# Optimization experiments

Hardware: AMD Instinct MI355X
Metric: run time of the kernel (lower is better)

The kernel has to match this reference:

```python
import jax, jax.numpy as jnp
import numpy as np

N, T, H, W, C = 64, 32, 64, 64, 256
HID, NB, P, OUT = 512, 12, 7, 388
CIN = P * P + 2  # 49 patch values + 2 normalized coords


def _ln(x, s):
    # haiku LayerNorm(axis=-1, create_scale=True, create_offset=False), eps=1e-5
    m = jnp.mean(x, axis=-1, keepdims=True)
    v = jnp.var(x, axis=-1, keepdims=True)
    return (x - m) * jax.lax.rsqrt(v + 1e-5) * s


def _dwconv(x, w, b, groups):
    # hk.DepthwiseConv1D, NWC, stride 1, SAME padding; w: [K, 1, C_out]
    y = jax.lax.conv_general_dilated(
        x, w, (1,), 'SAME', dimension_numbers=('NWC', 'WIO', 'NWC'),
        feature_group_count=groups)
    return y + b


def _forward(feature_grid, query_feats, pos, in_w, in_b, dw1_w, dw1_b, dw2_w,
             dw2_b, ln1_s, ln2_s, up_w, up_b, down_w, down_b, lnf_s, out_w,
             out_b):
    pad = P - 1
    # cost volume: einsum('bnc,bthwc->tbnhw') with batch=1, laid out [N,T,H,W]
    corrs = jnp.einsum('nc,thwc->nthw', query_feats, feature_grid)
    padded = jnp.pad(corrs, ((0, 0), (0, 0), (pad, pad), (pad, pad)))
    # extract_patch_depthwise_conv: the separable bilinear bump kernel convolved
    # VALID over the padded map equals a bilinear sample at (o + pos + P/2 - 1).
    pp = pos + P / 2.0 - 1.0  # [N,T,2] (y,x)
    iy = jnp.floor(pp[..., 0])
    ix = jnp.floor(pp[..., 1])
    fy = (pp[..., 0] - iy)[..., None, None]
    fx = (pp[..., 1] - ix)[..., None, None]
    offs = jnp.arange(P, dtype=jnp.int32)
    y0 = iy.astype(jnp.int32)[..., None] + offs  # [N,T,P]
    x0 = ix.astype(jnp.int32)[..., None] + offs  # [N,T,P]
    gat = jax.vmap(jax.vmap(lambda img, yi, xi: img[yi][:, xi]))
    patch = ((1 - fy) * (1 - fx) * gat(padded, y0, x0)
             + (1 - fy) * fx * gat(padded, y0, x0 + 1)
             + fy * (1 - fx) * gat(padded, y0 + 1, x0)
             + fy * fx * gat(padded, y0 + 1, x0 + 1))  # [N,T,P,P]
    x = jnp.concatenate(
        [patch.reshape(patch.shape[0], patch.shape[1], P * P),
         pos / jnp.float32(H)], axis=-1)  # [N,T,CIN]
    # PIPSMLPMixer
    x = x @ in_w + in_b  # [N,T,HID]
    for i in range(NB):
        # PIPsConvBlock: depthwise_conv_residual
        skip = x
        h = _ln(x, ln1_s[i])
        h = jax.nn.gelu(_dwconv(h, dw1_w[i], dw1_b[i], HID))  # ch mult 4
        h = _dwconv(h, dw2_w[i], dw2_b[i], HID * 4)           # ch mult 1
        h = h[..., 0::4] + h[..., 1::4] + h[..., 2::4] + h[..., 3::4]
        x = h + skip
        # conv_channels_mixer
        skip = x
        h = _ln(x, ln2_s[i])
        h = jax.nn.gelu(h @ up_w[i] + up_b[i]) @ down_w[i] + down_b[i]
        x = h + skip
    x = _ln(x, lnf_s)
    return x @ out_w + out_b  # [N,T,OUT]


def setup_inputs() -> dict:
    key = jax.random.key(0)
    ks = jax.random.split(key, 12)
    s = 0.02
    return dict(
        feature_grid=jax.random.normal(ks[0], (T, H, W, C), jnp.float32),
        query_feats=jax.random.normal(ks[1], (N, C), jnp.float32),
        pos=jax.random.uniform(ks[2], (N, T, 2), jnp.float32) * (H - 8),
        in_w=jax.random.normal(ks[3], (CIN, HID), jnp.float32) * s,
        in_b=jnp.zeros((HID,), jnp.float32),
        dw1_w=jax.random.normal(ks[4], (NB, 3, 1, HID * 4), jnp.float32) * s,
        dw1_b=jnp.zeros((NB, HID * 4), jnp.float32),
        dw2_w=jax.random.normal(ks[5], (NB, 3, 1, HID * 4), jnp.float32) * s,
        dw2_b=jnp.zeros((NB, HID * 4), jnp.float32),
        ln1_s=jnp.ones((NB, HID), jnp.float32),
        ln2_s=jnp.ones((NB, HID), jnp.float32),
        up_w=jax.random.normal(ks[6], (NB, HID, HID * 4), jnp.float32) * s,
        up_b=jnp.zeros((NB, HID * 4), jnp.float32),
        down_w=jax.random.normal(ks[7], (NB, HID * 4, HID), jnp.float32) * s,
        down_b=jnp.zeros((NB, HID), jnp.float32),
        lnf_s=jnp.ones((HID,), jnp.float32),
        out_w=jax.random.normal(ks[8], (HID, OUT), jnp.float32) * s,
        out_b=jnp.zeros((OUT,), jnp.float32),
    )


def reference(feature_grid, query_feats, pos, in_w, in_b, dw1_w, dw1_b, dw2_w,
              dw2_b, ln1_s, ln2_s, up_w, up_b, down_w, down_b, lnf_s, out_w,
              out_b):
    return _forward(feature_grid, query_feats, pos, in_w, in_b, dw1_w, dw1_b,
                    dw2_w, dw2_b, ln1_s, ln2_s, up_w, up_b, down_w, down_b,
                    lnf_s, out_w, out_b)
```

## Files before the change

kernel.cpp:

```cpp
#include <hip/hip_runtime.h>
#include <hip/hip_bf16.h>

#define N_    64
#define T_    32
#define H_    64
#define W_    64
#define C_    256
#define HID   512
#define HID4  2048
#define NBLK  12
#define P_    7
#define OUT_  388
#define OUTP  448
#define CIN   51
#define M_    (N_*T_)

typedef __attribute__((ext_vector_type(4))) float f32x4;
typedef __attribute__((ext_vector_type(8))) short bf16x8;

__device__ __forceinline__ float gelu_f(float x) {
    float x3 = x * x * x;
    return 0.5f * x * (1.f + tanhf(0.7978845608028654f * (x + 0.044715f * x3)));
}

__device__ __forceinline__ void gload_lds16(const void* g, void* l) {
    __builtin_amdgcn_global_load_lds(
        (const __attribute__((address_space(1))) void*)g,
        (__attribute__((address_space(3))) void*)l, 16, 0, 0);
}

__global__ __launch_bounds__(256) void patch_kernel(
    const float* __restrict__ fg, const float* __restrict__ qf,
    const float* __restrict__ pos, const float* __restrict__ in_w,
    const float* __restrict__ in_b, float* __restrict__ x) {
    __shared__ float4 q[64];
    __shared__ float g[8][8];
    __shared__ float xrow[CIN];
    int m = blockIdx.x;
    int n = m >> 5;
    int t = m & (T_ - 1);
    int tid = threadIdx.x, wid = tid >> 6, lane = tid & 63;
    if (tid < 64) q[tid] = *(const float4*)&qf[n * C_ + tid * 4];
    __syncthreads();
    float posy = pos[m * 2 + 0];
    float posx = pos[m * 2 + 1];
    float py = posy + 2.5f;
    float px = posx + 2.5f;
    int iy = (int)floorf(py), ix = (int)floorf(px);
    float fy = py - (float)iy, fx = px - (float)ix;
    float4 qv = q[lane];
    #pragma unroll
    for (int i = 0; i < 16; ++i) {
        int idx = wid * 16 + i;
        int a = idx >> 3, b = idx & 7;
        int y = iy + a - 6, xc = ix + b - 6;
        float partial = 0.f;
        if (y >= 0 && y < H_ && xc >= 0 && xc < W_) {
            const float4* fp = (const float4*)&fg[(((t * H_ + y) * W_) + xc) * C_];
            float4 v = fp[lane];
            partial = v.x * qv.x + v.y * qv.y + v.z * qv.z + v.w * qv.w;
        }
        #pragma unroll
        for (int o2 = 32; o2; o2 >>= 1) partial += __shfl_xor(partial, o2);
        if (lane == 0) g[a][b] = partial;
    }
    __syncthreads();
    if (tid < 49) {
        int p = tid / 7, qq = tid % 7;
        xrow[tid] = (1.f - fy) * (1.f - fx) * g[p][qq]
                  + (1.f - fy) * fx         * g[p][qq + 1]
                  + fy         * (1.f - fx) * g[p + 1][qq]
                  + fy         * fx         * g[p + 1][qq + 1];
    } else if (tid == 49) {
        xrow[49] = posy * (1.f / 64.f);
    } else if (tid == 50) {
        xrow[50] = posx * (1.f / 64.f);
    }
    __syncthreads();
    float acc0 = in_b[tid], acc1 = in_b[tid + 256];
    #pragma unroll
    for (int c = 0; c < CIN; ++c) {
        float rv = xrow[c];
        acc0 += rv * in_w[c * HID + tid];
        acc1 += rv * in_w[c * HID + tid + 256];
    }
    x[m * HID + tid] = acc0;
    x[m * HID + tid + 256] = acc1;
}

__global__ __launch_bounds__(512) void fused_dw_kernel(
    const float* __restrict__ xin, float* __restrict__ xout,
    __hip_bfloat16* __restrict__ t1b,
    const float* __restrict__ ln1s, const float* __restrict__ ln2s,
    const float* __restrict__ w1, const float* __restrict__ b1,
    const float* __restrict__ w2, const float* __restrict__ b2) {
    __shared__ float2 part[12][8];
    int n = blockIdx.y;
    int t0 = blockIdx.x * 8;
    int j = threadIdx.x;
    int lane = j & 63, wave = j >> 6;

    float xv[12];
    #pragma unroll
    for (int tt = 0; tt < 12; ++tt) {
        int t = t0 - 2 + tt;
        xv[tt] = (t >= 0 && t < T_) ? xin[(n * T_ + t) * HID + j] : 0.f;
    }
    #pragma unroll
    for (int tt = 0; tt < 12; ++tt) {
        float s = xv[tt], q = xv[tt] * xv[tt];
        #pragma unroll
        for (int o = 32; o; o >>= 1) { s += __shfl_xor(s, o); q += __shfl_xor(q, o); }
        if (lane == 0) part[tt][wave] = make_float2(s, q);
    }
    __syncthreads();
    float s1v = ln1s[j];
    float xl[12];
    #pragma unroll
    for (int tt = 0; tt < 12; ++tt) {
        int t = t0 - 2 + tt;
        if (t >= 0 && t < T_) {
            float s = 0.f, q = 0.f;
            #pragma unroll
            for (int w = 0; w < 8; ++w) { float2 p = part[tt][w]; s += p.x; q += p.y; }
            float mean = s * (1.f / HID);
            float var  = q * (1.f / HID) - mean * mean;
            xl[tt] = (xv[tt] - mean) * rsqrtf(var + 1e-5f) * s1v;
        } else xl[tt] = 0.f;
    }
    float w1a[12], w2a[12], b1a[4];
    #pragma unroll
    for (int r = 0; r < 3; ++r) {
        *(float4*)&w1a[r * 4] = *(const float4*)&w1[r * HID4 + 4 * j];
        *(float4*)&w2a[r * 4] = *(const float4*)&w2[r * HID4 + 4 * j];
    }
    *(float4*)&b1a[0] = *(const float4*)&b1[4 * j];
    float4 b2v = *(const float4*)&b2[4 * j];
    float h[8];
    float b2sum = b2v.x + b2v.y + b2v.z + b2v.w;
    #pragma unroll
    for (int i = 0; i < 8; ++i) h[i] = b2sum;
    #pragma unroll
    for (int k = 0; k < 4; ++k) {
        float gk[10];
        #pragma unroll
        for (int idx = 0; idx < 10; ++idx) {
            int tp = t0 - 1 + idx;
            if (tp >= 0 && tp < T_) {
                float a = b1a[k] + w1a[0 * 4 + k] * xl[idx]
                                 + w1a[1 * 4 + k] * xl[idx + 1]
                                 + w1a[2 * 4 + k] * xl[idx + 2];
                gk[idx] = gelu_f(a);
            } else gk[idx] = 0.f;
        }
        #pragma unroll
        for (int i = 0; i < 8; ++i)
            h[i] += w2a[0 * 4 + k] * gk[i] + w2a[1 * 4 + k] * gk[i + 1]
                  + w2a[2 * 4 + k] * gk[i + 2];
    }
    float xn[8];
    #pragma unroll
    for (int i = 0; i < 8; ++i) xn[i] = xv[i + 2] + h[i];
    __syncthreads();
    #pragma unroll
    for (int i = 0; i < 8; ++i) {
        float s = xn[i], q = xn[i] * xn[i];
        #pragma unroll
        for (int o = 32; o; o >>= 1) { s += __shfl_xor(s, o); q += __shfl_xor(q, o); }
        if (lane == 0) part[i][wave] = make_float2(s, q);
    }
    __syncthreads();
    float s2v = ln2s[j];
    #pragma unroll
    for (int i = 0; i < 8; ++i) {
        float s = 0.f, q = 0.f;
        #pragma unroll
        for (int w = 0; w < 8; ++w) { float2 p = part[i][w]; s += p.x; q += p.y; }
        float mean = s * (1.f / HID);
        float var  = q * (1.f / HID) - mean * mean;
        float rstd = rsqrtf(var + 1e-5f);
        int m = (n * T_ + t0 + i) * HID + j;
        xout[m] = xn[i];
        t1b[m] = __float2bfloat16((xn[i] - mean) * rstd * s2v);
    }
}

__global__ __launch_bounds__(256) void ln_kernel(
    const float* __restrict__ in, const float* __restrict__ s,
    __hip_bfloat16* __restrict__ outb) {
    int wid = threadIdx.x >> 6, lane = threadIdx.x & 63;
    int row = blockIdx.x * 4 + wid;
    const float* r = in + row * HID + lane * 8;
    float4 v0 = *(const float4*)r;
    float4 v1 = *(const float4*)(r + 4);
    float sum = v0.x + v0.y + v0.z + v0.w + v1.x + v1.y + v1.z + v1.w;
    float sq  = v0.x*v0.x + v0.y*v0.y + v0.z*v0.z + v0.w*v0.w
              + v1.x*v1.x + v1.y*v1.y + v1.z*v1.z + v1.w*v1.w;
    #pragma unroll
    for (int o = 32; o; o >>= 1) { sum += __shfl_xor(sum, o); sq += __shfl_xor(sq, o); }
    float mean = sum * (1.f / HID);
    float var  = sq * (1.f / HID) - mean * mean;
    float rstd = rsqrtf(var + 1e-5f);
    const float* sp = s + lane * 8;
    float4 s0 = *(const float4*)sp;
    float4 s1 = *(const float4*)(sp + 4);
    float o[8];
    o[0] = (v0.x - mean) * rstd * s0.x; o[1] = (v0.y - mean) * rstd * s0.y;
    o[2] = (v0.z - mean) * rstd * s0.z; o[3] = (v0.w - mean) * rstd * s0.w;
    o[4] = (v1.x - mean) * rstd * s1.x; o[5] = (v1.y - mean) * rstd * s1.y;
    o[6] = (v1.z - mean) * rstd * s1.z; o[7] = (v1.w - mean) * rstd * s1.w;
    alignas(16) __hip_bfloat16 tmp[8];
    #pragma unroll
    for (int i = 0; i < 8; ++i) tmp[i] = __float2bfloat16(o[i]);
    *(bf16x8*)&outb[row * HID + lane * 8] = *(bf16x8*)tmp;
}

__global__ __launch_bounds__(256) void tcvt_kernel(
    const float* __restrict__ src, __hip_bfloat16* __restrict__ dst,
    int R, int C, int Cpad) {
    __shared__ float tile[32][33];
    size_t zb = blockIdx.z;
    src += zb * (size_t)R * C;
    dst += zb * (size_t)Cpad * R;
    int c0 = blockIdx.x * 32, r0 = blockIdx.y * 32;
    int tx = threadIdx.x & 31, ty = threadIdx.x >> 5;
    #pragma unroll
    for (int i = 0; i < 4; ++i) {
        int r = r0 + ty + i * 8, c = c0 + tx;
        tile[ty + i * 8][tx] = (c < C) ? src[(size_t)r * C + c] : 0.f;
    }
    __syncthreads();
    #pragma unroll
    for (int i = 0; i < 4; ++i) {
        int c = c0 + ty + i * 8, r = r0 + tx;
        dst[(size_t)c * R + r] = __float2bfloat16(tile[tx][ty + i * 8]);
    }
}

template <int BM, int BN, int FM, int FN, int EPI>
__global__ __launch_bounds__(256) void gemm_mfma(
    const __hip_bfloat16* __restrict__ A, const __hip_bfloat16* __restrict__ Bt,
    const float* __restrict__ bias, float* __restrict__ Cf,
    __hip_bfloat16* __restrict__ Cb, int K, int ldN, int Nstore) {
    constexpr int LOADS = BM / 32 + BN / 32;
    __shared__ alignas(16) __hip_bfloat16 As[3][BM * 64];
    __shared__ alignas(16) __hip_bfloat16 Bs[3][BN * 64];
    int tid = threadIdx.x;
    int lane = tid & 63, wave = tid >> 6;
    int wr = wave >> 1, wc = wave & 1;
    int row0 = blockIdx.y * BM, col0 = blockIdx.x * BN;

    f32x4 acc[FM][FN];
    #pragma unroll
    for (int m = 0; m < FM; ++m)
        #pragma unroll
        for (int n = 0; n < FN; ++n)
            acc[m][n] = (f32x4){0.f, 0.f, 0.f, 0.f};

    int rI = lane >> 3;
    int cp = lane & 7;

    auto stage = [&](int buf, int k0) {
        #pragma unroll
        for (int s = 0; s < BM / 32; ++s) {
            int rbase = wave * (BM / 4) + s * 8;
            int row = rbase + rI;
            int corig = cp ^ (row & 7);
            gload_lds16(A + (size_t)(row0 + row) * K + k0 + corig * 8,
                        (char*)As[buf] + rbase * 128);
        }
        #pragma unroll
        for (int s = 0; s < BN / 32; ++s) {
            int rbase = wave * (BN / 4) + s * 8;
            int row = rbase + rI;
            int corig = cp ^ (row & 7);
            gload_lds16(Bt + (size_t)(col0 + row) * K + k0 + corig * 8,
                        (char*)Bs[buf] + rbase * 128);
        }
    };

    int nsteps = K >> 6;
    stage(0, 0);
    stage(1, 64);
    for (int step = 0; step < nsteps; ++step) {
        int cur = step % 3;
        if (step + 1 < nsteps) {
            asm volatile("s_waitcnt vmcnt(%0)" :: "n"(LOADS) : "memory");
        } else {
            asm volatile("s_waitcnt vmcnt(0)" ::: "memory");
        }
        __builtin_amdgcn_s_barrier();
        __builtin_amdgcn_sched_barrier(0);
        if (step + 2 < nsteps) stage((step + 2) % 3, (step + 2) * 64);
        #pragma unroll
        for (int kk = 0; kk < 2; ++kk) {
            bf16x8 af[FM], bfr[FN];
            #pragma unroll
            for (int m = 0; m < FM; ++m) {
                int row = wr * FM * 16 + m * 16 + (lane & 15);
                int chunk = (kk * 4 + (lane >> 4)) ^ (row & 7);
                af[m] = *(const bf16x8*)((const char*)As[cur] + row * 128 + chunk * 16);
            }
            #pragma unroll
            for (int n = 0; n < FN; ++n) {
                int row = wc * FN * 16 + n * 16 + (lane & 15);
                int chunk = (kk * 4 + (lane >> 4)) ^ (row & 7);
                bfr[n] = *(const bf16x8*)((const char*)Bs[cur] + row * 128 + chunk * 16);
            }
            __builtin_amdgcn_s_setprio(1);
            #pragma unroll
            for (int m = 0; m < FM; ++m)
                #pragma unroll
                for (int n = 0; n < FN; ++n)
                    acc[m][n] = __builtin_amdgcn_mfma_f32_16x16x32_bf16(
                        af[m], bfr[n], acc[m][n], 0, 0, 0);
            __builtin_amdgcn_s_setprio(0);
        }
    }

    int cr = (lane >> 4) * 4;
    int cc = lane & 15;
    #pragma unroll
    for (int m = 0; m < FM; ++m) {
        #pragma unroll
        for (int n = 0; n < FN; ++n) {
            #pragma unroll
            for (int j = 0; j < 4; ++j) {
                int row = row0 + wr * FM * 16 + m * 16 + cr + j;
                int col = col0 + wc * FN * 16 + n * 16 + cc;
                float v = acc[m][n][j];
                if (EPI == 0) {
                    if (col < Nstore)
                        Cf[(size_t)row * Nstore + col] = v + bias[col];
                } else if (EPI == 1) {
                    v = gelu_f(v + bias[col]);
                    Cb[(size_t)row * ldN + col] = __float2bfloat16(v);
                } else {
                    Cf[(size_t)row * ldN + col] += v + bias[col];
                }
            }
        }
    }
}

extern "C" void kernel_launch(void* const* d_in, const int* in_sizes, int n_in,
                              void* d_out, int out_size, void* d_ws, size_t ws_size,
                              hipStream_t stream) {
    const float* fg     = (const float*)d_in[0];
    const float* qf     = (const float*)d_in[1];
    const float* pos    = (const float*)d_in[2];
    const float* in_w   = (const float*)d_in[3];
    const float* in_b   = (const float*)d_in[4];
    const float* dw1_w  = (const float*)d_in[5];
    const float* dw1_b  = (const float*)d_in[6];
    const float* dw2_w  = (const float*)d_in[7];
    const float* dw2_b  = (const float*)d_in[8];
    const float* ln1_s  = (const float*)d_in[9];
    const float* ln2_s  = (const float*)d_in[10];
    const float* up_w   = (const float*)d_in[11];
    const float* up_b   = (const float*)d_in[12];
    const float* down_w = (const float*)d_in[13];
    const float* down_b = (const float*)d_in[14];
    const float* lnf_s  = (const float*)d_in[15];
    const float* out_w  = (const float*)d_in[16];
    const float* out_b  = (const float*)d_in[17];
    float* out = (float*)d_out;

    char* ws = (char*)d_ws;
    float* xa = (float*)ws;                        ws += (size_t)M_ * HID * 4;
    float* xb = (float*)ws;                        ws += (size_t)M_ * HID * 4;
    __hip_bfloat16* t1b = (__hip_bfloat16*)ws;     ws += (size_t)M_ * HID * 2;
    __hip_bfloat16* t2b = (__hip_bfloat16*)ws;     ws += (size_t)M_ * HID4 * 2;
    __hip_bfloat16* upT  = (__hip_bfloat16*)ws;    ws += (size_t)NBLK * HID4 * HID * 2;
    __hip_bfloat16* dnT  = (__hip_bfloat16*)ws;    ws += (size_t)NBLK * HID * HID4 * 2;
    __hip_bfloat16* outT = (__hip_bfloat16*)ws;    ws += (size_t)OUTP * HID * 2;

    tcvt_kernel<<<dim3(HID4 / 32, HID / 32, NBLK), 256, 0, stream>>>(
        up_w, upT, HID, HID4, HID4);
    tcvt_kernel<<<dim3(HID / 32, HID4 / 32, NBLK), 256, 0, stream>>>(
        down_w, dnT, HID4, HID, HID);
    tcvt_kernel<<<dim3(OUTP / 32, HID / 32, 1), 256, 0, stream>>>(
        out_w, outT, HID, OUT_, OUTP);

    patch_kernel<<<M_, 256, 0, stream>>>(fg, qf, pos, in_w, in_b, xa);

    float* xc = xa;
    float* xn = xb;
    for (int b = 0; b < NBLK; ++b) {
        fused_dw_kernel<<<dim3(4, N_), 512, 0, stream>>>(
            xc, xn, t1b, ln1_s + b * HID, ln2_s + b * HID,
            dw1_w + b * 3 * HID4, dw1_b + b * HID4,
            dw2_w + b * 3 * HID4, dw2_b + b * HID4);
        gemm_mfma<128, 64, 4, 2, 1><<<dim3(HID4 / 64, M_ / 128), 256, 0, stream>>>(
            t1b, upT + (size_t)b * HID4 * HID, up_b + b * HID4, nullptr, t2b,
            HID, HID4, HID4);
        gemm_mfma<64, 64, 2, 2, 2><<<dim3(HID / 64, M_ / 64), 256, 0, stream>>>(
            t2b, dnT + (size_t)b * HID * HID4, down_b + b * HID, xn, nullptr,
            HID4, HID, HID);
        float* tmp = xc; xc = xn; xn = tmp;
    }

    ln_kernel<<<M_ / 4, 256, 0, stream>>>(xc, lnf_s, t1b);
    gemm_mfma<128, 64, 4, 2, 0><<<dim3(OUTP / 64, M_ / 128), 256, 0, stream>>>(
        t1b, outT, out_b, out, nullptr, HID, OUT_, OUT_);
}
```

Measured before the change: 735.6 us.

## Use 64x64 GEMM tiles with intra-block split-K for down projection

Replaces the templated GEMM with a fixed 64x64-tile kernel that switches from triple to double buffering. The kernel can split K across two 4-wave groups in one 512-thread block and reduce the partial sums through shared memory. The up and output projections now use 64-row tiles, which doubles their block count. The down projection (K=2048, only 256 blocks) uses split-K to put more waves on each tile. The cost is a shallower prefetch pipeline, an extra LDS reduction and barrier, and less register-level reuse per wave in the up GEMM.

```diff
diff --git a/kernel.cpp b/kernel.cpp
--- a/kernel.cpp
+++ b/kernel.cpp
@@ -237,24 +237,27 @@
     }
 }
 
-template <int BM, int BN, int FM, int FN, int EPI>
-__global__ __launch_bounds__(256) void gemm_mfma(
+template <int KG, int EPI>
+__global__ __launch_bounds__(256 * KG) void gemm64(
     const __hip_bfloat16* __restrict__ A, const __hip_bfloat16* __restrict__ Bt,
     const float* __restrict__ bias, float* __restrict__ Cf,
     __hip_bfloat16* __restrict__ Cb, int K, int ldN, int Nstore) {
-    constexpr int LOADS = BM / 32 + BN / 32;
-    __shared__ alignas(16) __hip_bfloat16 As[3][BM * 64];
-    __shared__ alignas(16) __hip_bfloat16 Bs[3][BN * 64];
+    __shared__ alignas(16) __hip_bfloat16 As[KG][2][64 * 64];
+    __shared__ alignas(16) __hip_bfloat16 Bs[KG][2][64 * 64];
     int tid = threadIdx.x;
     int lane = tid & 63, wave = tid >> 6;
-    int wr = wave >> 1, wc = wave & 1;
-    int row0 = blockIdx.y * BM, col0 = blockIdx.x * BN;
-
-    f32x4 acc[FM][FN];
-    #pragma unroll
-    for (int m = 0; m < FM; ++m)
-        #pragma unroll
-        for (int n = 0; n < FN; ++n)
+    int g = wave >> 2;
+    int w4 = wave & 3;
+    int wr = w4 >> 1, wc = w4 & 1;
+    int row0 = blockIdx.y * 64, col0 = blockIdx.x * 64;
+    int Kg = K / KG;
+    int kbase = g * Kg;
+
+    f32x4 acc[2][2];
+    #pragma unroll
+    for (int m = 0; m < 2; ++m)
+        #pragma unroll
+        for (int n = 0; n < 2; ++n)
             acc[m][n] = (f32x4){0.f, 0.f, 0.f, 0.f};
 
     int rI = lane >> 3;
@@ -262,56 +265,57 @@
 
     auto stage = [&](int buf, int k0) {
         #pragma unroll
-        for (int s = 0; s < BM / 32; ++s) {
-            int rbase = wave * (BM / 4) + s * 8;
+        for (int s = 0; s < 2; ++s) {
+            int rbase = w4 * 16 + s * 8;
             int row = rbase + rI;
             int corig = cp ^ (row & 7);
-            gload_lds16(A + (size_t)(row0 + row) * K + k0 + corig * 8,
-                        (char*)As[buf] + rbase * 128);
-        }
-        #pragma unroll
-        for (int s = 0; s < BN / 32; ++s) {
-            int rbase = wave * (BN / 4) + s * 8;
+            gload_lds16(A + (size_t)(row0 + row) * K + kbase + k0 + corig * 8,
+                        (char*)As[g][buf] + rbase * 128);
+        }
+        #pragma unroll
+        for (int s = 0; s < 2; ++s) {
+            int rbase = w4 * 16 + s * 8;
             int row = rbase + rI;
             int corig = cp ^ (row & 7);
-            gload_lds16(Bt + (size_t)(col0 + row) * K + k0 + corig * 8,
-                        (char*)Bs[buf] + rbase * 128);
+            gload_lds16(Bt + (size_t)(col0 + row) * K + kbase + k0 + corig * 8,
+                        (char*)Bs[g][buf] + rbase * 128);
         }
     };
 
-    int nsteps = K >> 6;
+    int nsteps = Kg >> 6;
     stage(0, 0);
-    stage(1, 64);
     for (int step = 0; step < nsteps; ++step) {
-        int cur = step % 3;
+        int cur = step & 1;
+        __builtin_amdgcn_s_barrier();
         if (step + 1 < nsteps) {
-            asm volatile("s_waitcnt vmcnt(%0)" :: "n"(LOADS) : "memory");
+            stage(cur ^ 1, (step + 1) * 64);
+            asm volatile("s_waitcnt vmcnt(4)" ::: "memory");
         } else {
             asm volatile("s_waitcnt vmcnt(0)" ::: "memory");
         }
+        __builtin_amdgcn_sched_barrier(0);
         __builtin_amdgcn_s_barrier();
         __builtin_amdgcn_sched_barrier(0);
-        if (step + 2 < nsteps) stage((step + 2) % 3, (step + 2) * 64);
         #pragma unroll
         for (int kk = 0; kk < 2; ++kk) {
-            bf16x8 af[FM], bfr[FN];
-            #pragma unroll
-            for (int m = 0; m < FM; ++m) {
-                int row = wr * FM * 16 + m * 16 + (lane & 15);
+            bf16x8 af[2], bfr[2];
+            #pragma unroll
+            for (int m = 0; m < 2; ++m) {
+                int row = wr * 32 + m * 16 + (lane & 15);
                 int chunk = (kk * 4 + (lane >> 4)) ^ (row & 7);
-                af[m] = *(const bf16x8*)((const char*)As[cur] + row * 128 + chunk * 16);
+                af[m] = *(const bf16x8*)((const char*)As[g][cur] + row * 128 + chunk * 16);
             }
             #pragma unroll
-            for (int n = 0; n < FN; ++n) {
-                int row = wc * FN * 16 + n * 16 + (lane & 15);
+            for (int n = 0; n < 2; ++n) {
+                int row = wc * 32 + n * 16 + (lane & 15);
                 int chunk = (kk * 4 + (lane >> 4)) ^ (row & 7);
-                bfr[n] = *(const bf16x8*)((const char*)Bs[cur] + row * 128 + chunk * 16);
+                bfr[n] = *(const bf16x8*)((const char*)Bs[g][cur] + row * 128 + chunk * 16);
             }
             __builtin_amdgcn_s_setprio(1);
             #pragma unroll
-            for (int m = 0; m < FM; ++m)
+            for (int m = 0; m < 2; ++m)
                 #pragma unroll
-                for (int n = 0; n < FN; ++n)
+                for (int n = 0; n < 2; ++n)
                     acc[m][n] = __builtin_amdgcn_mfma_f32_16x16x32_bf16(
                         af[m], bfr[n], acc[m][n], 0, 0, 0);
             __builtin_amdgcn_s_setprio(0);
@@ -320,14 +324,40 @@
 
     int cr = (lane >> 4) * 4;
     int cc = lane & 15;
-    #pragma unroll
-    for (int m = 0; m < FM; ++m) {
-        #pragma unroll
-        for (int n = 0; n < FN; ++n) {
+
+    if (KG == 2) {
+        float* scratch = (float*)&As[0][0][0];
+        __syncthreads();
+        if (g == 1) {
+            #pragma unroll
+            for (int m = 0; m < 2; ++m)
+                #pragma unroll
+                for (int n = 0; n < 2; ++n)
+                    #pragma unroll
+                    for (int j = 0; j < 4; ++j)
+                        scratch[(wr * 32 + m * 16 + cr + j) * 64 +
+                                wc * 32 + n * 16 + cc] = acc[m][n][j];
+        }
+        __syncthreads();
+        if (g == 1) return;
+        #pragma unroll
+        for (int m = 0; m < 2; ++m)
+            #pragma unroll
+            for (int n = 0; n < 2; ++n)
+                #pragma unroll
+                for (int j = 0; j < 4; ++j)
+                    acc[m][n][j] += scratch[(wr * 32 + m * 16 + cr + j) * 64 +
+                                            wc * 32 + n * 16 + cc];
+    }
+
+    #pragma unroll
+    for (int m = 0; m < 2; ++m) {
+        #pragma unroll
+        for (int n = 0; n < 2; ++n) {
             #pragma unroll
             for (int j = 0; j < 4; ++j) {
-                int row = row0 + wr * FM * 16 + m * 16 + cr + j;
-                int col = col0 + wc * FN * 16 + n * 16 + cc;
+                int row = row0 + wr * 32 + m * 16 + cr + j;
+                int col = col0 + wc * 32 + n * 16 + cc;
                 float v = acc[m][n][j];
                 if (EPI == 0) {
                     if (col < Nstore)
@@ -391,16 +421,16 @@
             xc, xn, t1b, ln1_s + b * HID, ln2_s + b * HID,
             dw1_w + b * 3 * HID4, dw1_b + b * HID4,
             dw2_w + b * 3 * HID4, dw2_b + b * HID4);
-        gemm_mfma<128, 64, 4, 2, 1><<<dim3(HID4 / 64, M_ / 128), 256, 0, stream>>>(
+        gemm64<1, 1><<<dim3(HID4 / 64, M_ / 64), 256, 0, stream>>>(
             t1b, upT + (size_t)b * HID4 * HID, up_b + b * HID4, nullptr, t2b,
             HID, HID4, HID4);
-        gemm_mfma<64, 64, 2, 2, 2><<<dim3(HID / 64, M_ / 64), 256, 0, stream>>>(
+        gemm64<2, 2><<<dim3(HID / 64, M_ / 64), 512, 0, stream>>>(
             t2b, dnT + (size_t)b * HID * HID4, down_b + b * HID, xn, nullptr,
             HID4, HID, HID);
         float* tmp = xc; xc = xn; xn = tmp;
     }
 
     ln_kernel<<<M_ / 4, 256, 0, stream>>>(xc, lnf_s, t1b);
-    gemm_mfma<128, 64, 4, 2, 0><<<dim3(OUTP / 64, M_ / 128), 256, 0, stream>>>(
+    gemm64<1, 0><<<dim3(OUTP / 64, M_ / 64), 256, 0, stream>>>(
         t1b, outT, out_b, out, nullptr, HID, OUT_, OUT_);
 }
```

Result: faster. 640.3 us (-13.0%).
